# Performance work log

Hardware: AMD Instinct MI355X
Metric: run time of the kernel (lower is better)

## Reference

```python
import jax, jax.numpy as jnp
import numpy as np

M, B, D, N = 8, 200000, 32, 100000
TINY = np.finfo(np.float32).tiny


def _vol(box):
    # box: (..., 2, D) with box[...,0,:]=z (min corner), box[...,1,:]=Z (max corner)
    side = jnp.clip(box[..., 1, :] - box[..., 0, :], 0.0, None)
    return jnp.prod(side, axis=-1)


def _intersection(a, b):
    z = jnp.maximum(a[..., 0, :], b[..., 0, :])
    Z = jnp.minimum(a[..., 1, :], b[..., 1, :])
    return jnp.stack((z, Z), axis=-2)


def setup_inputs() -> dict:
    key = jax.random.key(0)
    k1, k2, k3, k4 = jax.random.split(key, 4)
    z = jax.random.uniform(k1, (M, B, 1, D), dtype=jnp.float32) * 0.1
    Z = 0.9 + jax.random.uniform(k2, (M, B, 1, D), dtype=jnp.float32) * 0.1
    box_param = jnp.concatenate([z, Z], axis=2)  # (M, B, 2, D)
    weights = jax.random.normal(k3, (M,), dtype=jnp.float32)
    ids = jax.random.randint(k4, (N, 4), 0, B, dtype=jnp.int64)
    return {"box_param": box_param, "weights": weights, "ids": ids}


def reference(box_param, weights, ids):
    boxes = jnp.clip(box_param, 0.0, 1.0)  # default universe -> clamp to [0,1]
    w = jax.nn.softmax(weights)            # (M,)
    # default universe box has volume prod(1-0) = 1
    uz = jnp.zeros((D,), boxes.dtype)
    uZ = jnp.ones((D,), boxes.dtype)
    universe_vol = _vol(jnp.stack((uz, uZ), axis=-2))  # scalar 1.0

    def wsum(vols):  # vols: (M, N) -> (N,)
        return jnp.einsum('m,mn->n', w, vols)

    i0, i1, i2 = ids[:, 0], ids[:, 1], ids[:, 2]
    A = boxes[:, i0]   # (M, N, 2, D)
    Bb = boxes[:, i1]
    C = boxes[:, i2]

    unary_probs = wsum(_vol(A) / universe_vol)

    AiB = _intersection(A, Bb)
    two_vol = wsum(_vol(AiB) / universe_vol) + TINY
    two_div = wsum(_vol(A) / universe_vol) + TINY
    two_cond = jnp.exp(jnp.log(two_vol) - jnp.log(two_div))

    three_vol = wsum(_vol(_intersection(AiB, C)) / universe_vol) + TINY
    three_div = wsum(_vol(AiB) / universe_vol) + TINY
    three_cond = jnp.exp(jnp.log(three_vol) - jnp.log(three_div))

    unary_mask = i0 == i1
    three_mask = i1 != i2
    two_mask = jnp.logical_and(~three_mask, ~unary_mask)
    # torch writes unary, then two, then three -> three takes precedence
    probs = jnp.where(three_mask, three_cond,
            jnp.where(two_mask, two_cond,
            jnp.where(unary_mask, unary_probs, 0.0)))
    return probs
```

## Files before the change

kernel.cpp:

```cpp
#include <hip/hip_runtime.h>
#include <hip/hip_bf16.h>


#define MM 8
#define BB 200000
#define DD 32

__global__ __launch_bounds__(256) void box_triples_kernel(
    const float* __restrict__ box,
    const float* __restrict__ wts,
    const int*   __restrict__ ids,
    float*       __restrict__ out,
    int N)
{
    const int lane = threadIdx.x & 63;
    const int wave = threadIdx.x >> 6;
    const int n = blockIdx.x * (blockDim.x >> 6) + wave;
    if (n >= N) return;

    const int m = lane >> 3;
    const int t = lane & 7;

    const int4 idv = ((const int4*)ids)[n];
    const int i0 = idv.x, i1 = idv.y, i2 = idv.z;

    const int baseA = (m * BB + i0) * (2 * DD) + t * 4;
    const int baseB = (m * BB + i1) * (2 * DD) + t * 4;
    const int baseC = (m * BB + i2) * (2 * DD) + t * 4;

    const float4 zA4 = *(const float4*)(box + baseA);
    const float4 ZA4 = *(const float4*)(box + baseA + DD);
    const float4 zB4 = *(const float4*)(box + baseB);
    const float4 ZB4 = *(const float4*)(box + baseB + DD);
    const float4 zC4 = *(const float4*)(box + baseC);
    const float4 ZC4 = *(const float4*)(box + baseC + DD);

    float wl = wts[m];
    float wmax = wl;
    #pragma unroll
    for (int off = 8; off < 64; off <<= 1) wmax = fmaxf(wmax, __shfl_xor(wmax, off));
    float ew = __expf(wl - wmax);
    float esum = ew;
    #pragma unroll
    for (int off = 8; off < 64; off <<= 1) esum += __shfl_xor(esum, off);
    const float w = ew / esum;

    float pA = 1.f, pAB = 1.f, pABC = 1.f;
    #define CL(x) fminf(fmaxf((x), 0.f), 1.f)
    #define COMP(c) { \
        const float za = CL(zA4.c), Za = CL(ZA4.c); \
        const float zb = CL(zB4.c), Zb = CL(ZB4.c); \
        const float zc = CL(zC4.c), Zc = CL(ZC4.c); \
        const float zab  = fmaxf(za, zb),  Zab  = fminf(Za, Zb); \
        const float zabc = fmaxf(zab, zc), Zabc = fminf(Zab, Zc); \
        pA   *= fmaxf(Za   - za,   0.f); \
        pAB  *= fmaxf(Zab  - zab,  0.f); \
        pABC *= fmaxf(Zabc - zabc, 0.f); \
    }
    COMP(x) COMP(y) COMP(z) COMP(w)
    #undef COMP
    #undef CL

    #pragma unroll
    for (int off = 1; off < 8; off <<= 1) {
        pA   *= __shfl_xor(pA,   off);
        pAB  *= __shfl_xor(pAB,  off);
        pABC *= __shfl_xor(pABC, off);
    }

    float sA = w * pA, sAB = w * pAB, sABC = w * pABC;
    #pragma unroll
    for (int off = 8; off < 64; off <<= 1) {
        sA   += __shfl_xor(sA,   off);
        sAB  += __shfl_xor(sAB,  off);
        sABC += __shfl_xor(sABC, off);
    }

    const float TINY = 1.1754943508222875e-38f;
    float res;
    if (i1 != i2) {
        res = (sABC + TINY) / (sAB + TINY);
    } else if (i0 != i1) {
        res = (sAB + TINY) / (sA + TINY);
    } else {
        res = sA;
    }

    if (lane == 0) out[n] = res;
}

extern "C" void kernel_launch(void* const* d_in, const int* in_sizes, int n_in,
                              void* d_out, int out_size, void* d_ws, size_t ws_size,
                              hipStream_t stream) {
    const float* box = (const float*)d_in[0];
    const float* wts = (const float*)d_in[1];
    const int*   ids = (const int*)d_in[2];
    float* out = (float*)d_out;
    const int N = out_size;

    const int wavesPerBlock = 4;
    const int blocks = (N + wavesPerBlock - 1) / wavesPerBlock;
    box_triples_kernel<<<blocks, 256, 0, stream>>>(box, wts, ids, out, N);
}
```

Measured before the change: 526.6 us.

## Split mixture components across grid and reduce partials in second kernel

Restructures the computation so each block handles one mixture component for 32 queries, writing weighted volume partials to a workspace, and a second kernel sums the components and applies the conditional-probability selection. This aims to change the gather access pattern and occupancy compared with one wave per query covering all components. It adds workspace traffic and an extra launch, and falls back to the old kernel if the workspace is too small.

```diff
diff --git a/kernel.cpp b/kernel.cpp
--- a/kernel.cpp
+++ b/kernel.cpp
@@ -1,10 +1,107 @@
 #include <hip/hip_runtime.h>
-#include <hip/hip_bf16.h>
 
 
 #define MM 8
 #define BB 200000
 #define DD 32
+
+__global__ __launch_bounds__(256) void box_triples_pass1(
+    const float* __restrict__ box,
+    const float* __restrict__ wts,
+    const int*   __restrict__ ids,
+    float*       __restrict__ ws,
+    int N)
+{
+    const int lane = threadIdx.x & 63;
+    const int wave = threadIdx.x >> 6;
+    const int m = blockIdx.y;
+    const int r = lane >> 3;
+    const int t = lane & 7;
+    const int n = (blockIdx.x * 4 + wave) * 8 + r;
+    if (n >= N) return;
+
+    const int4 idv = ((const int4*)ids)[n];
+    const int i0 = idv.x, i1 = idv.y, i2 = idv.z;
+
+    const int baseA = (m * BB + i0) * (2 * DD) + t * 4;
+    const int baseB = (m * BB + i1) * (2 * DD) + t * 4;
+    const int baseC = (m * BB + i2) * (2 * DD) + t * 4;
+
+    const float4 zA4 = *(const float4*)(box + baseA);
+    const float4 ZA4 = *(const float4*)(box + baseA + DD);
+    const float4 zB4 = *(const float4*)(box + baseB);
+    const float4 ZB4 = *(const float4*)(box + baseB + DD);
+    const float4 zC4 = *(const float4*)(box + baseC);
+    const float4 ZC4 = *(const float4*)(box + baseC + DD);
+
+    float mx = wts[0];
+    #pragma unroll
+    for (int k = 1; k < MM; ++k) mx = fmaxf(mx, wts[k]);
+    float s = 0.f;
+    #pragma unroll
+    for (int k = 0; k < MM; ++k) s += __expf(wts[k] - mx);
+    const float w = __expf(wts[m] - mx) / s;
+
+    float pA = 1.f, pAB = 1.f, pABC = 1.f;
+    #define CL(x) fminf(fmaxf((x), 0.f), 1.f)
+    #define COMP(c) { \
+        const float za = CL(zA4.c), Za = CL(ZA4.c); \
+        const float zb = CL(zB4.c), Zb = CL(ZB4.c); \
+        const float zc = CL(zC4.c), Zc = CL(ZC4.c); \
+        const float zab  = fmaxf(za, zb),  Zab  = fminf(Za, Zb); \
+        const float zabc = fmaxf(zab, zc), Zabc = fminf(Zab, Zc); \
+        pA   *= fmaxf(Za   - za,   0.f); \
+        pAB  *= fmaxf(Zab  - zab,  0.f); \
+        pABC *= fmaxf(Zabc - zabc, 0.f); \
+    }
+    COMP(x) COMP(y) COMP(z) COMP(w)
+    #undef COMP
+    #undef CL
+
+    #pragma unroll
+    for (int off = 1; off < 8; off <<= 1) {
+        pA   *= __shfl_xor(pA,   off);
+        pAB  *= __shfl_xor(pAB,  off);
+        pABC *= __shfl_xor(pABC, off);
+    }
+
+    if (t < 3) {
+        const float v = (t == 0) ? w * pA : (t == 1) ? w * pAB : w * pABC;
+        ws[(m * 3 + t) * N + n] = v;
+    }
+}
+
+__global__ __launch_bounds__(256) void box_triples_pass2(
+    const int*   __restrict__ ids,
+    const float* __restrict__ ws,
+    float*       __restrict__ out,
+    int N)
+{
+    const int n = blockIdx.x * 256 + threadIdx.x;
+    if (n >= N) return;
+
+    float sA = 0.f, sAB = 0.f, sABC = 0.f;
+    #pragma unroll
+    for (int m = 0; m < MM; ++m) {
+        sA   += ws[(m * 3 + 0) * N + n];
+        sAB  += ws[(m * 3 + 1) * N + n];
+        sABC += ws[(m * 3 + 2) * N + n];
+    }
+
+    const int4 idv = ((const int4*)ids)[n];
+    const int i0 = idv.x, i1 = idv.y, i2 = idv.z;
+
+    const float TINY = 1.1754943508222875e-38f;
+    float res;
+    if (i1 != i2) {
+        res = (sABC + TINY) / (sAB + TINY);
+    } else if (i0 != i1) {
+        res = (sAB + TINY) / (sA + TINY);
+    } else {
+        res = sA;
+    }
+    out[n] = res;
+}
 
 __global__ __launch_bounds__(256) void box_triples_kernel(
     const float* __restrict__ box,
@@ -98,7 +195,16 @@
     float* out = (float*)d_out;
     const int N = out_size;
 
-    const int wavesPerBlock = 4;
-    const int blocks = (N + wavesPerBlock - 1) / wavesPerBlock;
-    box_triples_kernel<<<blocks, 256, 0, stream>>>(box, wts, ids, out, N);
-}
+    const size_t ws_needed = (size_t)MM * 3 * N * sizeof(float);
+    if (ws_size >= ws_needed) {
+        float* ws = (float*)d_ws;
+        dim3 grid1((N + 31) / 32, MM);
+        box_triples_pass1<<<grid1, 256, 0, stream>>>(box, wts, ids, ws, N);
+        const int blocks2 = (N + 255) / 256;
+        box_triples_pass2<<<blocks2, 256, 0, stream>>>(ids, ws, out, N);
+    } else {
+        const int wavesPerBlock = 4;
+        const int blocks = (N + wavesPerBlock - 1) / wavesPerBlock;
+        box_triples_kernel<<<blocks, 256, 0, stream>>>(box, wts, ids, out, N);
+    }
+}
```

Result: no change. 520.5 us (-1.2%).

## Process eight queries per wave, looping over mixture components serially

Applied to the files above, without the earlier changes.

Each wave now handles eight queries (one per 8-lane group) instead of one, and every group loops over the 8 mixture components, keeping a running weighted sum in registers. This removes the cross-group shuffle reductions and the per-wave softmax shuffles, and the softmax is now computed redundantly per thread from the scalar weights. The work per thread grows eightfold with a serial dependency over components, so fewer waves are launched and latency hiding has to come from unroll 2 and occupancy. A 64-bit offset is used for the component stride.

```diff
diff --git a/kernel.cpp b/kernel.cpp
--- a/kernel.cpp
+++ b/kernel.cpp
@@ -1,12 +1,11 @@
 #include <hip/hip_runtime.h>
-#include <hip/hip_bf16.h>
 
 
 #define MM 8
 #define BB 200000
 #define DD 32
 
-__global__ __launch_bounds__(256) void box_triples_kernel(
+__global__ __launch_bounds__(256) void box_triples_fused(
     const float* __restrict__ box,
     const float* __restrict__ wts,
     const int*   __restrict__ ids,
@@ -15,65 +14,67 @@
 {
     const int lane = threadIdx.x & 63;
     const int wave = threadIdx.x >> 6;
-    const int n = blockIdx.x * (blockDim.x >> 6) + wave;
+    const int r = lane >> 3;
+    const int t = lane & 7;
+    const int n = (blockIdx.x * 4 + wave) * 8 + r;
     if (n >= N) return;
-
-    const int m = lane >> 3;
-    const int t = lane & 7;
 
     const int4 idv = ((const int4*)ids)[n];
     const int i0 = idv.x, i1 = idv.y, i2 = idv.z;
 
-    const int baseA = (m * BB + i0) * (2 * DD) + t * 4;
-    const int baseB = (m * BB + i1) * (2 * DD) + t * 4;
-    const int baseC = (m * BB + i2) * (2 * DD) + t * 4;
+    float mx = wts[0];
+    #pragma unroll
+    for (int k = 1; k < MM; ++k) mx = fmaxf(mx, wts[k]);
+    float s = 0.f;
+    #pragma unroll
+    for (int k = 0; k < MM; ++k) s += __expf(wts[k] - mx);
+    const float inv_s = 1.f / s;
 
-    const float4 zA4 = *(const float4*)(box + baseA);
-    const float4 ZA4 = *(const float4*)(box + baseA + DD);
-    const float4 zB4 = *(const float4*)(box + baseB);
-    const float4 ZB4 = *(const float4*)(box + baseB + DD);
-    const float4 zC4 = *(const float4*)(box + baseC);
-    const float4 ZC4 = *(const float4*)(box + baseC + DD);
+    const float* pa = box + i0 * (2 * DD) + t * 4;
+    const float* pb = box + i1 * (2 * DD) + t * 4;
+    const float* pc = box + i2 * (2 * DD) + t * 4;
 
-    float wl = wts[m];
-    float wmax = wl;
-    #pragma unroll
-    for (int off = 8; off < 64; off <<= 1) wmax = fmaxf(wmax, __shfl_xor(wmax, off));
-    float ew = __expf(wl - wmax);
-    float esum = ew;
-    #pragma unroll
-    for (int off = 8; off < 64; off <<= 1) esum += __shfl_xor(esum, off);
-    const float w = ew / esum;
+    float sA = 0.f, sAB = 0.f, sABC = 0.f;
 
-    float pA = 1.f, pAB = 1.f, pABC = 1.f;
-    #define CL(x) fminf(fmaxf((x), 0.f), 1.f)
-    #define COMP(c) { \
-        const float za = CL(zA4.c), Za = CL(ZA4.c); \
-        const float zb = CL(zB4.c), Zb = CL(ZB4.c); \
-        const float zc = CL(zC4.c), Zc = CL(ZC4.c); \
-        const float zab  = fmaxf(za, zb),  Zab  = fminf(Za, Zb); \
-        const float zabc = fmaxf(zab, zc), Zabc = fminf(Zab, Zc); \
-        pA   *= fmaxf(Za   - za,   0.f); \
-        pAB  *= fmaxf(Zab  - zab,  0.f); \
-        pABC *= fmaxf(Zabc - zabc, 0.f); \
-    }
-    COMP(x) COMP(y) COMP(z) COMP(w)
-    #undef COMP
-    #undef CL
+    #pragma unroll 2
+    for (int m = 0; m < MM; ++m) {
+        const size_t moff = (size_t)m * (BB * 2 * DD);
 
-    #pragma unroll
-    for (int off = 1; off < 8; off <<= 1) {
-        pA   *= __shfl_xor(pA,   off);
-        pAB  *= __shfl_xor(pAB,  off);
-        pABC *= __shfl_xor(pABC, off);
-    }
+        const float4 zA4 = *(const float4*)(pa + moff);
+        const float4 ZA4 = *(const float4*)(pa + moff + DD);
+        const float4 zB4 = *(const float4*)(pb + moff);
+        const float4 ZB4 = *(const float4*)(pb + moff + DD);
+        const float4 zC4 = *(const float4*)(pc + moff);
+        const float4 ZC4 = *(const float4*)(pc + moff + DD);
 
-    float sA = w * pA, sAB = w * pAB, sABC = w * pABC;
-    #pragma unroll
-    for (int off = 8; off < 64; off <<= 1) {
-        sA   += __shfl_xor(sA,   off);
-        sAB  += __shfl_xor(sAB,  off);
-        sABC += __shfl_xor(sABC, off);
+        const float w = __expf(wts[m] - mx) * inv_s;
+
+        float pA = 1.f, pAB = 1.f, pABC = 1.f;
+        #define CL(x) fminf(fmaxf((x), 0.f), 1.f)
+        #define COMP(c) { \
+            const float za = CL(zA4.c), Za = CL(ZA4.c); \
+            const float zb = CL(zB4.c), Zb = CL(ZB4.c); \
+            const float zc = CL(zC4.c), Zc = CL(ZC4.c); \
+            const float zab  = fmaxf(za, zb),  Zab  = fminf(Za, Zb); \
+            const float zabc = fmaxf(zab, zc), Zabc = fminf(Zab, Zc); \
+            pA   *= fmaxf(Za   - za,   0.f); \
+            pAB  *= fmaxf(Zab  - zab,  0.f); \
+            pABC *= fmaxf(Zabc - zabc, 0.f); \
+        }
+        COMP(x) COMP(y) COMP(z) COMP(w)
+        #undef COMP
+        #undef CL
+
+        #pragma unroll
+        for (int off = 1; off < 8; off <<= 1) {
+            pA   *= __shfl_xor(pA,   off);
+            pAB  *= __shfl_xor(pAB,  off);
+            pABC *= __shfl_xor(pABC, off);
+        }
+
+        sA   += w * pA;
+        sAB  += w * pAB;
+        sABC += w * pABC;
     }
 
     const float TINY = 1.1754943508222875e-38f;
@@ -86,7 +87,7 @@
         res = sA;
     }
 
-    if (lane == 0) out[n] = res;
+    if (t == 0) out[n] = res;
 }
 
 extern "C" void kernel_launch(void* const* d_in, const int* in_sizes, int n_in,
@@ -98,7 +99,6 @@
     float* out = (float*)d_out;
     const int N = out_size;
 
-    const int wavesPerBlock = 4;
-    const int blocks = (N + wavesPerBlock - 1) / wavesPerBlock;
-    box_triples_kernel<<<blocks, 256, 0, stream>>>(box, wts, ids, out, N);
+    const int blocks = (N + 31) / 32;
+    box_triples_fused<<<blocks, 256, 0, stream>>>(box, wts, ids, out, N);
 }
```

New measurement: 518.7 us. No clear change (-1.5%).
